# Kernel tuning notes

Hardware: AMD Instinct MI355X
Metric: run time of the kernel (lower is better)

## Reference

```python
import jax, jax.numpy as jnp
import numpy as np
import math

B, S, D, K = 8, 2048, 1024, 64
EPS = 1e-5

def _ln(x):
    m = jnp.mean(x, axis=-1, keepdims=True)
    v = jnp.mean((x - m) ** 2, axis=-1, keepdims=True)
    return (x - m) * jax.lax.rsqrt(v + EPS)

def setup_inputs() -> dict:
    key = jax.random.key(0)
    ks = jax.random.split(key, 14)
    s = 0.02
    return {
        "x":  jax.random.normal(ks[0], (B, S, D), dtype=jnp.float32),
        "Wk": jax.random.normal(ks[1], (D, K), dtype=jnp.float32) * s,
        "bk": jnp.zeros((K,), dtype=jnp.float32),
        "Wq": jax.random.normal(ks[2], (D, K), dtype=jnp.float32) * s,
        "bq": jnp.zeros((K,), dtype=jnp.float32),
        "Wv": jax.random.normal(ks[3], (D, D), dtype=jnp.float32) * s,
        "bv": jnp.zeros((D,), dtype=jnp.float32),
        "Wb": jax.random.normal(ks[4], (D, 1), dtype=jnp.float32) * s,
        "bb": jnp.zeros((1,), dtype=jnp.float32),
        "W1": jax.random.normal(ks[5], (D, D), dtype=jnp.float32) * s,
        "b1": jnp.zeros((D,), dtype=jnp.float32),
        "g1": jnp.ones((D,), dtype=jnp.float32),
        "be1": jnp.zeros((D,), dtype=jnp.float32),
    }

def reference(x, Wk, bk, Wq, bq, Wv, bv, Wb, bb, W1, b1, g1, be1):
    scale = 1.0 / math.sqrt(K)
    keys    = (jnp.einsum('bsd,dk->bsk', x, Wk) + bk) * scale   # [B,S,K]
    queries = jnp.einsum('bsd,dk->bsk', x, Wq) + bq             # [B,S,K]
    values  = jnp.einsum('bsd,de->bse', x, Wv) + bv             # [B,S,D]
    biases  = jnp.einsum('bsd,do->bso', x, Wb) + bb             # [B,S,1]
    # scores[b,i,j] = keys[b,i] . queries[b,j] + biases[b,i]
    scores = jax.nn.sigmoid(jnp.einsum('bik,bjk->bij', keys, queries) + biases)
    attention = jnp.einsum('bij,bjd->bid', scores, values)      # [B,S,D]
    res = _ln(x + attention) * g1 + be1
    feedforward = jax.nn.relu(jnp.einsum('bsd,de->bse', res, W1) + b1)
    return _ln(res + feedforward)
```

## Files before the change

kernel.cpp:

```cpp
#include <hip/hip_runtime.h>
#include <math.h>


typedef __bf16 bf16_t;
typedef __bf16 bf16x4_t __attribute__((ext_vector_type(4)));
typedef __bf16 bf16x8_t __attribute__((ext_vector_type(8)));
typedef float  f32x4    __attribute__((ext_vector_type(4)));

#define DEV static __device__ __forceinline__

DEV void gll16(const void* g, void* l) {
  __builtin_amdgcn_global_load_lds(
      (const __attribute__((address_space(1))) void*)g,
      (__attribute__((address_space(3))) void*)l, 16, 0, 0);
}

template <int MODE, int MFAST>
__global__ __launch_bounds__(512, 2) void gemm256(
    const bf16_t* __restrict__ A, const bf16_t* __restrict__ B,
    bf16_t* __restrict__ C, int K, int lda, int ldb, int ldc,
    long sAb, long sBb, long sCb, const float* __restrict__ aux0) {
  const int gx = gridDim.x, gy = gridDim.y;
  const int gxy = gx * gy;
  const int nwg = gxy * (int)gridDim.z;
  const int orig = blockIdx.x + gx * blockIdx.y + gxy * blockIdx.z;
  const int lid = (orig & 7) * (nwg >> 3) + (orig >> 3);
  const int bz = lid / gxy;
  const int rem = lid - bz * gxy;
  const int bx = MFAST ? (rem / gy) : (rem % gx);
  const int by = MFAST ? (rem % gy) : (rem / gx);

  A += (long)bz * sAb;
  B += (long)bz * sBb;
  const int m0 = by * 256, n0 = bx * 256;

  __shared__ bf16_t SM[65536];
#define ASH(b, h) (&SM[(((b)*2 + (h)) << 13)])
#define BSH(b, h) (&SM[32768 + (((b)*2 + (h)) << 13)])

  const int tid = threadIdx.x;
  const int wid = tid >> 6, l = tid & 63;
  const int wr = wid >> 2, wc = wid & 3;
  const int lr = l & 15, lh = l >> 4;

  const int sRow = tid >> 2;
  const int sSl = (tid & 3) ^ ((tid >> 3) & 3);
  const bf16_t* Asrc = A + (long)(m0 + sRow) * lda + sSl * 8;
  const bf16_t* Bsrc = B + (long)(n0 + sRow) * ldb + sSl * 8;
  const long aStep = (long)128 * lda, bStep = (long)128 * ldb;

#define STAGE_A(b, h, kt) do { \
    const bf16_t* s_ = Asrc + (kt) * 64 + (h) * 32; \
    gll16(s_,         ASH(b, h) + tid * 8); \
    gll16(s_ + aStep, ASH(b, h) + 4096 + tid * 8); } while (0)
#define STAGE_B(b, h, kt) do { \
    const bf16_t* s_ = Bsrc + (kt) * 64 + (h) * 32; \
    gll16(s_,         BSH(b, h) + tid * 8); \
    gll16(s_ + bStep, BSH(b, h) + 4096 + tid * 8); } while (0)

  const int sw = (lh ^ ((lr >> 1) & 3)) * 8;
  const int aOff = (wr * 128 + lr) * 32 + sw;
  const int bOff = (wc * 64 + lr) * 32 + sw;

  f32x4 acc[8][4] = {};
  const int NT = K >> 6;

  STAGE_A(0, 0, 0); STAGE_B(0, 0, 0); STAGE_A(0, 1, 0); STAGE_B(0, 1, 0);
  asm volatile("s_waitcnt vmcnt(4)" ::: "memory");
  __builtin_amdgcn_s_barrier();

#define PHASE_SYNC() do { \
    __builtin_amdgcn_sched_barrier(0); \
    __builtin_amdgcn_s_barrier(); \
    asm volatile("s_waitcnt lgkmcnt(0)" ::: "memory"); \
    __builtin_amdgcn_sched_barrier(0); } while (0)
#define MFMA_LO() do { \
    __builtin_amdgcn_s_setprio(1); \
    _Pragma("unroll") for (int m = 0; m < 4; ++m) \
    _Pragma("unroll") for (int n = 0; n < 4; ++n) \
      acc[m][n] = __builtin_amdgcn_mfma_f32_16x16x32_bf16(aF[m], bF[n], acc[m][n], 0, 0, 0); \
    __builtin_amdgcn_s_setprio(0); } while (0)
#define MFMA_HI() do { \
    __builtin_amdgcn_s_setprio(1); \
    _Pragma("unroll") for (int m = 0; m < 4; ++m) \
    _Pragma("unroll") for (int n = 0; n < 4; ++n) \
      acc[m + 4][n] = __builtin_amdgcn_mfma_f32_16x16x32_bf16(aG[m], bF[n], acc[m + 4][n], 0, 0, 0); \
    __builtin_amdgcn_s_setprio(0); } while (0)

  for (int t = 0; t < NT; ++t) {
    const int p = t & 1, q = p ^ 1;
    const bool pf = (t + 1 < NT);
    bf16x8_t bF[4], aF[4], aG[4];

#pragma unroll
    for (int n = 0; n < 4; ++n) bF[n] = *(const bf16x8_t*)(BSH(p, 0) + bOff + n * 512);
#pragma unroll
    for (int m = 0; m < 4; ++m) aF[m] = *(const bf16x8_t*)(ASH(p, 0) + aOff + m * 512);
    if (pf) STAGE_A(q, 0, t + 1);
    PHASE_SYNC();
    MFMA_LO();

#pragma unroll
    for (int m = 0; m < 4; ++m) aG[m] = *(const bf16x8_t*)(ASH(p, 0) + aOff + (m + 4) * 512);
    if (pf) {
      STAGE_B(q, 0, t + 1);
      asm volatile("s_waitcnt vmcnt(4)" ::: "memory");
    } else {
      asm volatile("s_waitcnt vmcnt(0)" ::: "memory");
    }
    PHASE_SYNC();
    MFMA_HI();

#pragma unroll
    for (int n = 0; n < 4; ++n) bF[n] = *(const bf16x8_t*)(BSH(p, 1) + bOff + n * 512);
#pragma unroll
    for (int m = 0; m < 4; ++m) aF[m] = *(const bf16x8_t*)(ASH(p, 1) + aOff + m * 512);
    if (pf) STAGE_A(q, 1, t + 1);
    PHASE_SYNC();
    MFMA_LO();

#pragma unroll
    for (int m = 0; m < 4; ++m) aG[m] = *(const bf16x8_t*)(ASH(p, 1) + aOff + (m + 4) * 512);
    if (pf) STAGE_B(q, 1, t + 1);
    asm volatile("s_waitcnt vmcnt(4)" ::: "memory");
    PHASE_SYNC();
    MFMA_HI();
  }
#undef STAGE_A
#undef STAGE_B
#undef PHASE_SYNC
#undef MFMA_LO
#undef MFMA_HI

  bf16_t* Cb = C + (long)bz * sCb;
  const int rowb = m0 + wr * 128 + lh * 4;
  const int colb = n0 + wc * 64 + lr;
#pragma unroll
  for (int m = 0; m < 8; ++m)
#pragma unroll
    for (int n = 0; n < 4; ++n) {
      const f32x4 v = acc[m][n];
      const int cc = colb + n * 16;
#pragma unroll
      for (int r = 0; r < 4; ++r) {
        const int rr = rowb + m * 16 + r;
        const float val = v[r];
        if constexpr (MODE == 1) {
          Cb[(long)rr * ldc + cc] = (bf16_t)(val + aux0[rr]);
        } else if constexpr (MODE == 3) {
          Cb[(long)rr * ldc + cc] = (bf16_t)val;
        } else {
          Cb[(long)rr * ldc + cc] = (bf16_t)fmaxf(val + aux0[cc], 0.0f);
        }
      }
    }
#undef ASH
#undef BSH
}

__global__ __launch_bounds__(256) void kq_thin(
    const bf16_t* __restrict__ A, const bf16_t* __restrict__ B,
    bf16_t* __restrict__ C,
    const float* __restrict__ bk, const float* __restrict__ bq) {
  const int m0 = blockIdx.x * 64;

  __shared__ bf16_t SM[12288];
#define ASH(b) (&SM[(b) << 11])
#define BSH(b) (&SM[4096 + ((b) << 12)])

  const int tid = threadIdx.x;
  const int w = tid >> 6, l = tid & 63;
  const int lr = l & 15, lh = l >> 4;

  const int sRow = tid >> 2;
  const int sSl = (tid & 3) ^ ((tid >> 3) & 3);
  const bf16_t* Asrc = A + (long)(m0 + sRow) * 1024 + sSl * 8;
  const bf16_t* Bsrc0 = B + (long)sRow * 1024 + sSl * 8;
  const bf16_t* Bsrc1 = B + (long)(64 + sRow) * 1024 + sSl * 8;

  const int sw = (lh ^ ((lr >> 1) & 3)) * 8;
  const int aOff = (w * 16 + lr) * 32 + sw;

  f32x4 acc[8] = {};

  auto stage = [&](int buf, int k0) {
    gll16(Asrc + k0, ASH(buf) + tid * 8);
    gll16(Bsrc0 + k0, BSH(buf) + tid * 8);
    gll16(Bsrc1 + k0, BSH(buf) + 2048 + tid * 8);
  };

  stage(0, 0);
  __syncthreads();
  int cur = 0;

  for (int k0 = 0; k0 < 1024; k0 += 32) {
    if (k0 + 32 < 1024) stage(cur ^ 1, k0 + 32);

    const bf16x8_t aF = *(const bf16x8_t*)(ASH(cur) + aOff);
    bf16x8_t bF[8];
#pragma unroll
    for (int j = 0; j < 8; ++j)
      bF[j] = *(const bf16x8_t*)(BSH(cur) + (j * 16 + lr) * 32 + sw);
#pragma unroll
    for (int j = 0; j < 8; ++j)
      acc[j] = __builtin_amdgcn_mfma_f32_16x16x32_bf16(aF, bF[j], acc[j], 0, 0, 0);

    __syncthreads();
    cur ^= 1;
  }

  {
#pragma unroll
    for (int j = 0; j < 8; ++j) {
      const f32x4 v = acc[j];
      const int cl = j * 16 + lr;
      const float b = (cl < 64) ? bk[cl] : bq[cl - 64];
      const float s = (cl < 64) ? 0.125f : 1.0f;
#pragma unroll
      for (int r = 0; r < 4; ++r) {
        const int rl = w * 16 + lh * 4 + r;
        SM[rl * 128 + (cl ^ (lh << 4))] = (bf16_t)((v[r] + b) * s);
      }
    }
    __syncthreads();
    const int chunk = tid & 15, rsub = tid >> 4;
#pragma unroll
    for (int pp = 0; pp < 4; ++pp) {
      const int rl = pp * 16 + rsub;
      const int sc = chunk ^ (((rl >> 2) & 3) << 1);
      const bf16x8_t vv = *(const bf16x8_t*)&SM[rl * 128 + sc * 8];
      *(bf16x8_t*)&C[(long)(m0 + rl) * 128 + chunk * 8] = vv;
    }
  }
#undef ASH
#undef BSH
}

template <int MODE, int MFAST>
__global__ __launch_bounds__(256) void gemm_bt(
    const bf16_t* __restrict__ A, const bf16_t* __restrict__ B,
    void* __restrict__ Cv, int M, int N, int K, int lda, int ldb, int ldc,
    long sAb, long sBb, long sCb,
    const float* __restrict__ aux0, const float* __restrict__ aux1, long sAux) {
  const int gx = gridDim.x, gy = gridDim.y;
  const int gxy = gx * gy;
  const int nwg = gxy * (int)gridDim.z;
  const int orig = blockIdx.x + gx * blockIdx.y + gxy * blockIdx.z;
  const int q = nwg >> 3, r8 = nwg & 7;
  const int xcd = orig & 7, seq = orig >> 3;
  const int lid = (xcd < r8 ? xcd * (q + 1) : r8 * (q + 1) + (xcd - r8) * q) + seq;
  const int bz = lid / gxy;
  const int rem = lid - bz * gxy;
  const int bx = MFAST ? (rem / gy) : (rem % gx);
  const int by = MFAST ? (rem % gy) : (rem / gx);

  A += (long)bz * sAb;
  B += (long)bz * sBb;
  const float* a0 = (MODE == 2) ? (aux0 + (long)bz * sAux) : aux0;

  const int m0 = by * 128;
  const int n0 = bx * 128;

  __shared__ bf16_t SM[16384];
#define ASH(b) (&SM[(b) << 12])
#define BSH(b) (&SM[8192 + ((b) << 12)])

  const int tid = threadIdx.x;
  const int w = tid >> 6, l = tid & 63;
  const int wr = w >> 1, wc = w & 1;
  const int lr = l & 15, lh = l >> 4;

  const int srow = l >> 2;
  const int scol = (((l & 3) ^ (srow & 3)) << 3);

  f32x4 acc[4][4] = {};

  auto stage = [&](int buf, int k0) {
#pragma unroll
    for (int half = 0; half < 2; ++half) {
      const int i = 2 * w + half;
      const int row = (i << 4) + srow;
      gll16(A + (long)(m0 + row) * lda + k0 + scol, ASH(buf) + (i << 9));
      gll16(B + (long)(n0 + row) * ldb + k0 + scol, BSH(buf) + (i << 9));
    }
  };

  stage(0, 0);
  __syncthreads();
  int cur = 0;
  const int sw = ((lh ^ (lr & 3)) << 3);

  for (int k0 = 0; k0 < K; k0 += 32) {
    if (k0 + 32 < K) stage(cur ^ 1, k0 + 32);

    bf16x8_t af[4], bfm[4];
#pragma unroll
    for (int m = 0; m < 4; ++m)
      af[m] = *(const bf16x8_t*)(ASH(cur) + (((wr << 6) + (m << 4) + lr) << 5) + sw);
#pragma unroll
    for (int n = 0; n < 4; ++n)
      bfm[n] = *(const bf16x8_t*)(BSH(cur) + (((wc << 6) + (n << 4) + lr) << 5) + sw);
#pragma unroll
    for (int m = 0; m < 4; ++m)
#pragma unroll
      for (int n = 0; n < 4; ++n)
        acc[m][n] = __builtin_amdgcn_mfma_f32_16x16x32_bf16(af[m], bfm[n], acc[m][n], 0, 0, 0);

    __syncthreads();
    cur ^= 1;
  }

  {
    const int rowb = (wr << 6) + (lh << 2);
    const int colb = (wc << 6) + lr;
#pragma unroll
    for (int m = 0; m < 4; ++m)
#pragma unroll
      for (int n = 0; n < 4; ++n) {
        const f32x4 v = acc[m][n];
        const int cl = colb + (n << 4);
#pragma unroll
        for (int r = 0; r < 4; ++r) {
          const int rl = rowb + (m << 4) + r;
          const float zz = v[r] + a0[m0 + rl];
          SM[rl * 128 + (cl ^ (lh << 4))] =
              (bf16_t)__builtin_amdgcn_rcpf(1.0f + __expf(-zz));
        }
      }
    __syncthreads();
    bf16_t* Cb = (bf16_t*)Cv + (long)bz * sCb;
    const int chunk = tid & 15, rsub = tid >> 4;
#pragma unroll
    for (int pp = 0; pp < 8; ++pp) {
      const int rl = pp * 16 + rsub;
      const int sc = chunk ^ (((rl >> 2) & 3) << 1);
      const bf16x8_t vv = *(const bf16x8_t*)&SM[rl * 128 + sc * 8];
      *(bf16x8_t*)&Cb[(long)(m0 + rl) * ldc + n0 + chunk * 8] = vv;
    }
  }
#undef ASH
#undef BSH
}

__global__ __launch_bounds__(256) void cast_bias_kernel(
    const float* __restrict__ x, const float* __restrict__ Wb,
    const float* __restrict__ bb, bf16_t* __restrict__ x_bf,
    float* __restrict__ biases) {
  const int r = blockIdx.x * 4 + (threadIdx.x >> 6);
  const int l = threadIdx.x & 63;
  const float* xr = x + (long)r * 1024;
  bf16_t* orow = x_bf + (long)r * 1024;
  float s = 0.f;
#pragma unroll
  for (int i = 0; i < 4; ++i) {
    const int off = l * 4 + i * 256;
    const float4 v = *(const float4*)(xr + off);
    const float4 w = *(const float4*)(Wb + off);
    s += v.x * w.x + v.y * w.y + v.z * w.z + v.w * w.w;
    bf16x4_t o;
    o[0] = (bf16_t)v.x; o[1] = (bf16_t)v.y; o[2] = (bf16_t)v.z; o[3] = (bf16_t)v.w;
    *(bf16x4_t*)(orow + off) = o;
  }
#pragma unroll
  for (int off = 1; off < 64; off <<= 1) s += __shfl_xor(s, off);
  if (l == 0) biases[r] = s + bb[0];
}

__global__ __launch_bounds__(256) void transpose_cast_kernel(
    const float* __restrict__ in, bf16_t* __restrict__ out, int R, int C) {
  __shared__ float t[32][33];
  const int c0 = blockIdx.x * 32, r0 = blockIdx.y * 32;
  const int tx = threadIdx.x & 31, ty = threadIdx.x >> 5;
#pragma unroll
  for (int i = 0; i < 4; ++i) {
    const int rl = ty * 4 + i;
    t[rl][tx] = in[(long)(r0 + rl) * C + c0 + tx];
  }
  __syncthreads();
#pragma unroll
  for (int i = 0; i < 4; ++i) {
    const int rl = ty * 4 + i;
    out[(long)(c0 + rl) * R + r0 + tx] = (bf16_t)t[tx][rl];
  }
}

DEV float2 block_sum2(float s, float ss) {
#pragma unroll
  for (int off = 1; off < 64; off <<= 1) {
    s += __shfl_xor(s, off);
    ss += __shfl_xor(ss, off);
  }
  __shared__ float bs[4], bss[4];
  const int w = threadIdx.x >> 6, l = threadIdx.x & 63;
  if (l == 0) { bs[w] = s; bss[w] = ss; }
  __syncthreads();
  s = bs[0] + bs[1] + bs[2] + bs[3];
  ss = bss[0] + bss[1] + bss[2] + bss[3];
  return make_float2(s, ss);
}

__global__ __launch_bounds__(256) void ln1_kernel(
    const bf16_t* __restrict__ x, const bf16_t* __restrict__ attn,
    const float* __restrict__ g, const float* __restrict__ be,
    bf16_t* __restrict__ res) {
  const long r = blockIdx.x;
  const int t = threadIdx.x;
  const bf16x4_t xv = *(const bf16x4_t*)(x + r * 1024 + t * 4);
  const bf16x4_t av = *(const bf16x4_t*)(attn + r * 1024 + t * 4);
  const float y0 = (float)xv[0] + (float)av[0], y1 = (float)xv[1] + (float)av[1];
  const float y2 = (float)xv[2] + (float)av[2], y3 = (float)xv[3] + (float)av[3];
  const float2 s2 = block_sum2(y0 + y1 + y2 + y3, y0 * y0 + y1 * y1 + y2 * y2 + y3 * y3);
  const float mean = s2.x * (1.0f / 1024.0f);
  const float var = s2.y * (1.0f / 1024.0f) - mean * mean;
  const float rs = rsqrtf(var + 1e-5f);
  const int c = t * 4;
  bf16x4_t o;
  o[0] = (bf16_t)((y0 - mean) * rs * g[c + 0] + be[c + 0]);
  o[1] = (bf16_t)((y1 - mean) * rs * g[c + 1] + be[c + 1]);
  o[2] = (bf16_t)((y2 - mean) * rs * g[c + 2] + be[c + 2]);
  o[3] = (bf16_t)((y3 - mean) * rs * g[c + 3] + be[c + 3]);
  *(bf16x4_t*)(res + r * 1024 + c) = o;
}

__global__ __launch_bounds__(256) void ln2_kernel(
    const bf16_t* __restrict__ res, const bf16_t* __restrict__ h,
    float* __restrict__ out) {
  const long r = blockIdx.x;
  const int t = threadIdx.x;
  const bf16x4_t rv = *(const bf16x4_t*)(res + r * 1024 + t * 4);
  const bf16x4_t hv = *(const bf16x4_t*)(h + r * 1024 + t * 4);
  const float y0 = (float)rv[0] + (float)hv[0], y1 = (float)rv[1] + (float)hv[1];
  const float y2 = (float)rv[2] + (float)hv[2], y3 = (float)rv[3] + (float)hv[3];
  const float2 s2 = block_sum2(y0 + y1 + y2 + y3, y0 * y0 + y1 * y1 + y2 * y2 + y3 * y3);
  const float mean = s2.x * (1.0f / 1024.0f);
  const float var = s2.y * (1.0f / 1024.0f) - mean * mean;
  const float rs = rsqrtf(var + 1e-5f);
  float4 o;
  o.x = (y0 - mean) * rs; o.y = (y1 - mean) * rs;
  o.z = (y2 - mean) * rs; o.w = (y3 - mean) * rs;
  ((float4*)(out + r * 1024))[t] = o;
}

extern "C" void kernel_launch(void* const* d_in, const int* in_sizes, int n_in,
                              void* d_out, int out_size, void* d_ws, size_t ws_size,
                              hipStream_t stream) {
  const float* x   = (const float*)d_in[0];
  const float* Wk  = (const float*)d_in[1];
  const float* bk  = (const float*)d_in[2];
  const float* Wq  = (const float*)d_in[3];
  const float* bq  = (const float*)d_in[4];
  const float* Wv  = (const float*)d_in[5];
  const float* bv  = (const float*)d_in[6];
  const float* Wb  = (const float*)d_in[7];
  const float* bb  = (const float*)d_in[8];
  const float* W1  = (const float*)d_in[9];
  const float* b1  = (const float*)d_in[10];
  const float* g1  = (const float*)d_in[11];
  const float* be1 = (const float*)d_in[12];
  float* out = (float*)d_out;

  char* ws = (char*)d_ws;
  bf16_t* x_bf    = (bf16_t*)(ws + 0);
  bf16_t* vt_bf   = (bf16_t*)(ws + 33554432);
  bf16_t* kq_bf   = (bf16_t*)(ws + 67108864);
  bf16_t* Wkqt    = (bf16_t*)(ws + 71303168);
  bf16_t* Wvt     = (bf16_t*)(ws + 71565312);
  bf16_t* W1t     = (bf16_t*)(ws + 73662464);
  float*  biases  = (float*) (ws + 75759616);
  bf16_t* scores  = (bf16_t*)(ws + 75825152);
  bf16_t* attn_bf = (bf16_t*)(ws + 142934016);
  bf16_t* res_bf  = (bf16_t*)(ws + 176488448);
  bf16_t* h_bf    = attn_bf;

  cast_bias_kernel<<<4096, 256, 0, stream>>>(x, Wb, bb, x_bf, biases);
  transpose_cast_kernel<<<dim3(2, 32), 256, 0, stream>>>(Wk, Wkqt, 1024, 64);
  transpose_cast_kernel<<<dim3(2, 32), 256, 0, stream>>>(Wq, Wkqt + 64 * 1024, 1024, 64);
  transpose_cast_kernel<<<dim3(32, 32), 256, 0, stream>>>(Wv, Wvt, 1024, 1024);
  transpose_cast_kernel<<<dim3(32, 32), 256, 0, stream>>>(W1, W1t, 1024, 1024);

  kq_thin<<<256, 256, 0, stream>>>(x_bf, Wkqt, kq_bf, bk, bq);

  gemm256<1, 1><<<dim3(64, 4, 1), 512, 0, stream>>>(
      Wvt, x_bf, vt_bf, 1024, 1024, 1024, 16384, 0, 0, 0, bv);

  gemm_bt<2, 0><<<dim3(16, 16, 8), 256, 0, stream>>>(
      kq_bf, kq_bf + 64, scores, 2048, 2048, 64, 128, 128, 2048,
      2048L * 128, 2048L * 128, 2048L * 2048, biases, nullptr, 2048);

  gemm256<3, 0><<<dim3(4, 8, 8), 512, 0, stream>>>(
      scores, vt_bf, attn_bf, 2048, 2048, 16384, 1024,
      2048L * 2048, 2048, 2048L * 1024, nullptr);

  ln1_kernel<<<16384, 256, 0, stream>>>(x_bf, attn_bf, g1, be1, res_bf);

  gemm256<4, 0><<<dim3(4, 64, 1), 512, 0, stream>>>(
      res_bf, W1t, h_bf, 1024, 1024, 1024, 1024, 0, 0, 0, b1);

  ln2_kernel<<<16384, 256, 0, stream>>>(res_bf, h_bf, out);
}
```

Measured before the change: 241.6 us.

## Switch gemm256 to 32x32x16 MFMA with full-K-tile staging; warp-per-row layernorms

The 256x256 GEMM now uses 32x32x16 bf16 MFMA instructions with 4x2 f32x16 accumulators instead of 16x16x32 with 8x4. It stages each whole 64-wide K tile at once with an 8-slot XOR swizzle and double buffering, split into four sub-phases. This cuts LDS read count per FLOP and simplifies the pipeline. Both layernorm kernels now process one row per wavefront with 16-byte vector loads and shuffle-only reductions, removing shared-memory block reductions and the syncthreads. The gemm_bt aux pointer now always adds the batch offset, which matters only for non-MODE-2 uses.

```diff
diff --git a/kernel.cpp b/kernel.cpp
--- a/kernel.cpp
+++ b/kernel.cpp
@@ -6,6 +6,7 @@
 typedef __bf16 bf16x4_t __attribute__((ext_vector_type(4)));
 typedef __bf16 bf16x8_t __attribute__((ext_vector_type(8)));
 typedef float  f32x4    __attribute__((ext_vector_type(4)));
+typedef float  f32x16   __attribute__((ext_vector_type(16)));
 
 #define DEV static __device__ __forceinline__
 
@@ -35,38 +36,41 @@
   const int m0 = by * 256, n0 = bx * 256;
 
   __shared__ bf16_t SM[65536];
-#define ASH(b, h) (&SM[(((b)*2 + (h)) << 13)])
-#define BSH(b, h) (&SM[32768 + (((b)*2 + (h)) << 13)])
+#define ASH(b) (&SM[(b) << 14])
+#define BSH(b) (&SM[32768 + ((b) << 14)])
 
   const int tid = threadIdx.x;
   const int wid = tid >> 6, l = tid & 63;
   const int wr = wid >> 2, wc = wid & 3;
-  const int lr = l & 15, lh = l >> 4;
-
-  const int sRow = tid >> 2;
-  const int sSl = (tid & 3) ^ ((tid >> 3) & 3);
-  const bf16_t* Asrc = A + (long)(m0 + sRow) * lda + sSl * 8;
-  const bf16_t* Bsrc = B + (long)(n0 + sRow) * ldb + sSl * 8;
-  const long aStep = (long)128 * lda, bStep = (long)128 * ldb;
-
-#define STAGE_A(b, h, kt) do { \
-    const bf16_t* s_ = Asrc + (kt) * 64 + (h) * 32; \
-    gll16(s_,         ASH(b, h) + tid * 8); \
-    gll16(s_ + aStep, ASH(b, h) + 4096 + tid * 8); } while (0)
-#define STAGE_B(b, h, kt) do { \
-    const bf16_t* s_ = Bsrc + (kt) * 64 + (h) * 32; \
-    gll16(s_,         BSH(b, h) + tid * 8); \
-    gll16(s_ + bStep, BSH(b, h) + 4096 + tid * 8); } while (0)
-
-  const int sw = (lh ^ ((lr >> 1) & 3)) * 8;
-  const int aOff = (wr * 128 + lr) * 32 + sw;
-  const int bOff = (wc * 64 + lr) * 32 + sw;
-
-  f32x4 acc[8][4] = {};
+  const int ln31 = l & 31, hi = l >> 5;
+
+  const int sRow = tid >> 3;
+  const int sSl = ((tid & 7) ^ ((tid >> 3) & 7)) << 3;
+  const bf16_t* Asrc = A + (long)(m0 + sRow) * lda + sSl;
+  const bf16_t* Bsrc = B + (long)(n0 + sRow) * ldb + sSl;
+  const long aStep = (long)64 * lda, bStep = (long)64 * ldb;
+
+#define STAGE_A(b, kt) do { \
+    const bf16_t* s_ = Asrc + (long)(kt) * 64; \
+    gll16(s_,             ASH(b) + tid * 8); \
+    gll16(s_ + aStep,     ASH(b) + 4096 + tid * 8); \
+    gll16(s_ + 2 * aStep, ASH(b) + 8192 + tid * 8); \
+    gll16(s_ + 3 * aStep, ASH(b) + 12288 + tid * 8); } while (0)
+#define STAGE_B(b, kt) do { \
+    const bf16_t* s_ = Bsrc + (long)(kt) * 64; \
+    gll16(s_,             BSH(b) + tid * 8); \
+    gll16(s_ + bStep,     BSH(b) + 4096 + tid * 8); \
+    gll16(s_ + 2 * bStep, BSH(b) + 8192 + tid * 8); \
+    gll16(s_ + 3 * bStep, BSH(b) + 12288 + tid * 8); } while (0)
+
+  const int aBase = (wr * 128 + ln31) * 64;
+  const int bBase = (wc * 64 + ln31) * 64;
+
+  f32x16 acc[4][2] = {};
   const int NT = K >> 6;
 
-  STAGE_A(0, 0, 0); STAGE_B(0, 0, 0); STAGE_A(0, 1, 0); STAGE_B(0, 1, 0);
-  asm volatile("s_waitcnt vmcnt(4)" ::: "memory");
+  STAGE_A(0, 0); STAGE_B(0, 0);
+  asm volatile("s_waitcnt vmcnt(0)" ::: "memory");
   __builtin_amdgcn_s_barrier();
 
 #define PHASE_SYNC() do { \
@@ -74,77 +78,49 @@
     __builtin_amdgcn_s_barrier(); \
     asm volatile("s_waitcnt lgkmcnt(0)" ::: "memory"); \
     __builtin_amdgcn_sched_barrier(0); } while (0)
-#define MFMA_LO() do { \
+
+#define PHASE(kk, ...) do { \
+    const int sl8 = ((((kk) << 1) | hi) ^ (l & 7)) << 3; \
+    _Pragma("unroll") for (int nf = 0; nf < 2; ++nf) \
+      bF[nf] = *(const bf16x8_t*)(BSH(p) + bBase + nf * 2048 + sl8); \
+    _Pragma("unroll") for (int mf = 0; mf < 4; ++mf) \
+      aF[mf] = *(const bf16x8_t*)(ASH(p) + aBase + mf * 2048 + sl8); \
+    __VA_ARGS__; \
+    PHASE_SYNC(); \
     __builtin_amdgcn_s_setprio(1); \
-    _Pragma("unroll") for (int m = 0; m < 4; ++m) \
-    _Pragma("unroll") for (int n = 0; n < 4; ++n) \
-      acc[m][n] = __builtin_amdgcn_mfma_f32_16x16x32_bf16(aF[m], bF[n], acc[m][n], 0, 0, 0); \
-    __builtin_amdgcn_s_setprio(0); } while (0)
-#define MFMA_HI() do { \
-    __builtin_amdgcn_s_setprio(1); \
-    _Pragma("unroll") for (int m = 0; m < 4; ++m) \
-    _Pragma("unroll") for (int n = 0; n < 4; ++n) \
-      acc[m + 4][n] = __builtin_amdgcn_mfma_f32_16x16x32_bf16(aG[m], bF[n], acc[m + 4][n], 0, 0, 0); \
+    _Pragma("unroll") for (int mf = 0; mf < 4; ++mf) \
+    _Pragma("unroll") for (int nf = 0; nf < 2; ++nf) \
+      acc[mf][nf] = __builtin_amdgcn_mfma_f32_32x32x16_bf16(aF[mf], bF[nf], acc[mf][nf], 0, 0, 0); \
     __builtin_amdgcn_s_setprio(0); } while (0)
 
   for (int t = 0; t < NT; ++t) {
     const int p = t & 1, q = p ^ 1;
     const bool pf = (t + 1 < NT);
-    bf16x8_t bF[4], aF[4], aG[4];
-
-#pragma unroll
-    for (int n = 0; n < 4; ++n) bF[n] = *(const bf16x8_t*)(BSH(p, 0) + bOff + n * 512);
-#pragma unroll
-    for (int m = 0; m < 4; ++m) aF[m] = *(const bf16x8_t*)(ASH(p, 0) + aOff + m * 512);
-    if (pf) STAGE_A(q, 0, t + 1);
-    PHASE_SYNC();
-    MFMA_LO();
-
-#pragma unroll
-    for (int m = 0; m < 4; ++m) aG[m] = *(const bf16x8_t*)(ASH(p, 0) + aOff + (m + 4) * 512);
-    if (pf) {
-      STAGE_B(q, 0, t + 1);
-      asm volatile("s_waitcnt vmcnt(4)" ::: "memory");
-    } else {
-      asm volatile("s_waitcnt vmcnt(0)" ::: "memory");
-    }
-    PHASE_SYNC();
-    MFMA_HI();
-
-#pragma unroll
-    for (int n = 0; n < 4; ++n) bF[n] = *(const bf16x8_t*)(BSH(p, 1) + bOff + n * 512);
-#pragma unroll
-    for (int m = 0; m < 4; ++m) aF[m] = *(const bf16x8_t*)(ASH(p, 1) + aOff + m * 512);
-    if (pf) STAGE_A(q, 1, t + 1);
-    PHASE_SYNC();
-    MFMA_LO();
-
-#pragma unroll
-    for (int m = 0; m < 4; ++m) aG[m] = *(const bf16x8_t*)(ASH(p, 1) + aOff + (m + 4) * 512);
-    if (pf) STAGE_B(q, 1, t + 1);
-    asm volatile("s_waitcnt vmcnt(4)" ::: "memory");
-    PHASE_SYNC();
-    MFMA_HI();
+    bf16x8_t aF[4], bF[2];
+
+    PHASE(0, { if (pf) { STAGE_A(q, t + 1); STAGE_B(q, t + 1); } });
+    PHASE(1, {});
+    PHASE(2, {});
+    PHASE(3, { asm volatile("s_waitcnt vmcnt(0)" ::: "memory"); });
   }
 #undef STAGE_A
 #undef STAGE_B
 #undef PHASE_SYNC
-#undef MFMA_LO
-#undef MFMA_HI
+#undef PHASE
 
   bf16_t* Cb = C + (long)bz * sCb;
-  const int rowb = m0 + wr * 128 + lh * 4;
-  const int colb = n0 + wc * 64 + lr;
-#pragma unroll
-  for (int m = 0; m < 8; ++m)
-#pragma unroll
-    for (int n = 0; n < 4; ++n) {
-      const f32x4 v = acc[m][n];
-      const int cc = colb + n * 16;
-#pragma unroll
-      for (int r = 0; r < 4; ++r) {
-        const int rr = rowb + m * 16 + r;
-        const float val = v[r];
+  const int rowb = m0 + wr * 128 + 4 * hi;
+  const int colb = n0 + wc * 64 + ln31;
+#pragma unroll
+  for (int mf = 0; mf < 4; ++mf)
+#pragma unroll
+    for (int nf = 0; nf < 2; ++nf) {
+      const f32x16 v = acc[mf][nf];
+      const int cc = colb + nf * 32;
+#pragma unroll
+      for (int reg = 0; reg < 16; ++reg) {
+        const int rr = rowb + mf * 32 + (reg & 3) + 8 * (reg >> 2);
+        const float val = v[reg];
         if constexpr (MODE == 1) {
           Cb[(long)rr * ldc + cc] = (bf16_t)(val + aux0[rr]);
         } else if constexpr (MODE == 3) {
@@ -256,7 +232,7 @@
 
   A += (long)bz * sAb;
   B += (long)bz * sBb;
-  const float* a0 = (MODE == 2) ? (aux0 + (long)bz * sAux) : aux0;
+  const float* a0 = aux0 + (long)bz * sAux;
 
   const int m0 = by * 128;
   const int n0 = bx * 128;
@@ -384,61 +360,87 @@
   }
 }
 
-DEV float2 block_sum2(float s, float ss) {
-#pragma unroll
-  for (int off = 1; off < 64; off <<= 1) {
-    s += __shfl_xor(s, off);
-    ss += __shfl_xor(ss, off);
-  }
-  __shared__ float bs[4], bss[4];
-  const int w = threadIdx.x >> 6, l = threadIdx.x & 63;
-  if (l == 0) { bs[w] = s; bss[w] = ss; }
-  __syncthreads();
-  s = bs[0] + bs[1] + bs[2] + bs[3];
-  ss = bss[0] + bss[1] + bss[2] + bss[3];
-  return make_float2(s, ss);
-}
-
 __global__ __launch_bounds__(256) void ln1_kernel(
     const bf16_t* __restrict__ x, const bf16_t* __restrict__ attn,
     const float* __restrict__ g, const float* __restrict__ be,
     bf16_t* __restrict__ res) {
-  const long r = blockIdx.x;
-  const int t = threadIdx.x;
-  const bf16x4_t xv = *(const bf16x4_t*)(x + r * 1024 + t * 4);
-  const bf16x4_t av = *(const bf16x4_t*)(attn + r * 1024 + t * 4);
-  const float y0 = (float)xv[0] + (float)av[0], y1 = (float)xv[1] + (float)av[1];
-  const float y2 = (float)xv[2] + (float)av[2], y3 = (float)xv[3] + (float)av[3];
-  const float2 s2 = block_sum2(y0 + y1 + y2 + y3, y0 * y0 + y1 * y1 + y2 * y2 + y3 * y3);
-  const float mean = s2.x * (1.0f / 1024.0f);
-  const float var = s2.y * (1.0f / 1024.0f) - mean * mean;
-  const float rs = rsqrtf(var + 1e-5f);
-  const int c = t * 4;
-  bf16x4_t o;
-  o[0] = (bf16_t)((y0 - mean) * rs * g[c + 0] + be[c + 0]);
-  o[1] = (bf16_t)((y1 - mean) * rs * g[c + 1] + be[c + 1]);
-  o[2] = (bf16_t)((y2 - mean) * rs * g[c + 2] + be[c + 2]);
-  o[3] = (bf16_t)((y3 - mean) * rs * g[c + 3] + be[c + 3]);
-  *(bf16x4_t*)(res + r * 1024 + c) = o;
+  const int w = threadIdx.x >> 6, l = threadIdx.x & 63;
+  const long r = (long)blockIdx.x * 4 + w;
+  const bf16_t* xr = x + r * 1024;
+  const bf16_t* ar = attn + r * 1024;
+  float y[16];
+  float s = 0.f, ss = 0.f;
+#pragma unroll
+  for (int h = 0; h < 2; ++h) {
+    const int base = h * 512 + l * 8;
+    const bf16x8_t xv = *(const bf16x8_t*)(xr + base);
+    const bf16x8_t av = *(const bf16x8_t*)(ar + base);
+#pragma unroll
+    for (int j = 0; j < 8; ++j) {
+      const float yy = (float)xv[j] + (float)av[j];
+      y[h * 8 + j] = yy;
+      s += yy; ss += yy * yy;
+    }
+  }
+#pragma unroll
+  for (int off = 1; off < 64; off <<= 1) {
+    s += __shfl_xor(s, off);
+    ss += __shfl_xor(ss, off);
+  }
+  const float mean = s * (1.0f / 1024.0f);
+  const float rs = rsqrtf(ss * (1.0f / 1024.0f) - mean * mean + 1e-5f);
+  bf16_t* orow = res + r * 1024;
+#pragma unroll
+  for (int h = 0; h < 2; ++h) {
+    const int base = h * 512 + l * 8;
+    bf16x8_t o;
+#pragma unroll
+    for (int j = 0; j < 8; ++j)
+      o[j] = (bf16_t)((y[h * 8 + j] - mean) * rs * g[base + j] + be[base + j]);
+    *(bf16x8_t*)(orow + base) = o;
+  }
 }
 
 __global__ __launch_bounds__(256) void ln2_kernel(
-    const bf16_t* __restrict__ res, const bf16_t* __restrict__ h,
+    const bf16_t* __restrict__ res, const bf16_t* __restrict__ hh,
     float* __restrict__ out) {
-  const long r = blockIdx.x;
-  const int t = threadIdx.x;
-  const bf16x4_t rv = *(const bf16x4_t*)(res + r * 1024 + t * 4);
-  const bf16x4_t hv = *(const bf16x4_t*)(h + r * 1024 + t * 4);
-  const float y0 = (float)rv[0] + (float)hv[0], y1 = (float)rv[1] + (float)hv[1];
-  const float y2 = (float)rv[2] + (float)hv[2], y3 = (float)rv[3] + (float)hv[3];
-  const float2 s2 = block_sum2(y0 + y1 + y2 + y3, y0 * y0 + y1 * y1 + y2 * y2 + y3 * y3);
-  const float mean = s2.x * (1.0f / 1024.0f);
-  const float var = s2.y * (1.0f / 1024.0f) - mean * mean;
-  const float rs = rsqrtf(var + 1e-5f);
-  float4 o;
-  o.x = (y0 - mean) * rs; o.y = (y1 - mean) * rs;
-  o.z = (y2 - mean) * rs; o.w = (y3 - mean) * rs;
-  ((float4*)(out + r * 1024))[t] = o;
+  const int w = threadIdx.x >> 6, l = threadIdx.x & 63;
+  const long r = (long)blockIdx.x * 4 + w;
+  const bf16_t* rr = res + r * 1024;
+  const bf16_t* hr = hh + r * 1024;
+  float y[16];
+  float s = 0.f, ss = 0.f;
+#pragma unroll
+  for (int h = 0; h < 2; ++h) {
+    const int base = h * 512 + l * 8;
+    const bf16x8_t rv = *(const bf16x8_t*)(rr + base);
+    const bf16x8_t hv = *(const bf16x8_t*)(hr + base);
+#pragma unroll
+    for (int j = 0; j < 8; ++j) {
+      const float yy = (float)rv[j] + (float)hv[j];
+      y[h * 8 + j] = yy;
+      s += yy; ss += yy * yy;
+    }
+  }
+#pragma unroll
+  for (int off = 1; off < 64; off <<= 1) {
+    s += __shfl_xor(s, off);
+    ss += __shfl_xor(ss, off);
+  }
+  const float mean = s * (1.0f / 1024.0f);
+  const float rs = rsqrtf(ss * (1.0f / 1024.0f) - mean * mean + 1e-5f);
+  float* orow = out + r * 1024;
+#pragma unroll
+  for (int h = 0; h < 2; ++h) {
+    const int base = h * 512 + l * 8;
+    float4 o1, o2;
+    o1.x = (y[h * 8 + 0] - mean) * rs; o1.y = (y[h * 8 + 1] - mean) * rs;
+    o1.z = (y[h * 8 + 2] - mean) * rs; o1.w = (y[h * 8 + 3] - mean) * rs;
+    o2.x = (y[h * 8 + 4] - mean) * rs; o2.y = (y[h * 8 + 5] - mean) * rs;
+    o2.z = (y[h * 8 + 6] - mean) * rs; o2.w = (y[h * 8 + 7] - mean) * rs;
+    *(float4*)(orow + base) = o1;
+    *(float4*)(orow + base + 4) = o2;
+  }
 }
 
 extern "C" void kernel_launch(void* const* d_in, const int* in_sizes, int n_in,
@@ -491,10 +493,10 @@
       scores, vt_bf, attn_bf, 2048, 2048, 16384, 1024,
       2048L * 2048, 2048, 2048L * 1024, nullptr);
 
-  ln1_kernel<<<16384, 256, 0, stream>>>(x_bf, attn_bf, g1, be1, res_bf);
+  ln1_kernel<<<4096, 256, 0, stream>>>(x_bf, attn_bf, g1, be1, res_bf);
 
   gemm256<4, 0><<<dim3(4, 64, 1), 512, 0, stream>>>(
       res_bf, W1t, h_bf, 1024, 1024, 1024, 1024, 0, 0, 0, b1);
 
-  ln2_kernel<<<16384, 256, 0, stream>>>(res_bf, h_bf, out);
-}
+  ln2_kernel<<<4096, 256, 0, stream>>>(res_bf, h_bf, out);
+}
```

Result: slower. 246.6 us (+2.1%).
